# Performance work log

Hardware: AMD Instinct MI355X
Metric: run time of the kernel (lower is better)

The kernel has to match this reference:

```python
import jax, jax.numpy as jnp
import numpy as np

D = 131072   # input_dim = 2*256*256
H = 512      # lstm_hidden_dim
OUT = 128    # out_dim


def _lstm_cell(x, h, c, W_ih, W_hh, b_ih, b_hh):
    # PyTorch LSTMCell: gates in order (i, f, g, o)
    gates = x @ W_ih.T + b_ih + h @ W_hh.T + b_hh  # [1, 4H]
    i, f, g, o = jnp.split(gates, 4, axis=-1)
    i = jax.nn.sigmoid(i)
    f = jax.nn.sigmoid(f)
    g = jnp.tanh(g)
    o = jax.nn.sigmoid(o)
    c_new = f * c + i * g
    h_new = o * jnp.tanh(c_new)
    return h_new, c_new


def setup_inputs() -> dict:
    key = jax.random.key(0)
    ks = jax.random.split(key, 20)
    s_ih = 1.0 / np.sqrt(H)
    inp = {
        "dL_dU": jax.random.normal(ks[0], (256, 256), jnp.float32),
        "dL_dV": jax.random.normal(ks[1], (256, 256), jnp.float32),
        "hidden": jax.random.normal(ks[2], (2, 1, H), jnp.float32),
        "cell": jax.random.normal(ks[3], (2, 1, H), jnp.float32),
        "W_ih1": jax.random.uniform(ks[4], (4 * H, D), jnp.float32, -s_ih, s_ih),
        "W_hh1": jax.random.uniform(ks[5], (4 * H, H), jnp.float32, -s_ih, s_ih),
        "b_ih1": jax.random.uniform(ks[6], (4 * H,), jnp.float32, -s_ih, s_ih),
        "b_hh1": jax.random.uniform(ks[7], (4 * H,), jnp.float32, -s_ih, s_ih),
        "W_ih2": jax.random.uniform(ks[8], (4 * H, H), jnp.float32, -s_ih, s_ih),
        "W_hh2": jax.random.uniform(ks[9], (4 * H, H), jnp.float32, -s_ih, s_ih),
        "b_ih2": jax.random.uniform(ks[10], (4 * H,), jnp.float32, -s_ih, s_ih),
        "b_hh2": jax.random.uniform(ks[11], (4 * H,), jnp.float32, -s_ih, s_ih),
        "W1": jax.random.uniform(ks[12], (OUT * OUT, H), jnp.float32, -s_ih, s_ih),
        "b1": jax.random.uniform(ks[13], (OUT * OUT,), jnp.float32, -s_ih, s_ih),
        "W2": jax.random.uniform(ks[14], (1, H), jnp.float32, -s_ih, s_ih),
        "b2": jax.random.uniform(ks[15], (1,), jnp.float32, -s_ih, s_ih),
        "W3": jax.random.uniform(ks[16], (1, H), jnp.float32, -s_ih, s_ih),
        "b3": jax.random.uniform(ks[17], (1,), jnp.float32, -s_ih, s_ih),
    }
    return inp


def reference(dL_dU, dL_dV, hidden, cell,
              W_ih1, W_hh1, b_ih1, b_hh1,
              W_ih2, W_hh2, b_ih2, b_hh2,
              W1, b1, W2, b2, W3, b3):
    grad_flat = jnp.concatenate([dL_dU.reshape(-1), dL_dV.reshape(-1)], axis=0)[None, :]  # [1, D]
    h0, c0 = _lstm_cell(grad_flat, hidden[0], cell[0], W_ih1, W_hh1, b_ih1, b_hh1)
    h1, c1 = _lstm_cell(h0, hidden[1], cell[1], W_ih2, W_hh2, b_ih2, b_hh2)
    g = (h1 @ W1.T + b1).reshape(OUT, OUT)
    step_size = jnp.clip(h1 @ W2.T + b2, 1e-07, 0.005)
    m_c = jnp.clip(2.0 * jnp.clip(h0 @ W3.T + b3, 0.0, 1.0), 0.0, 1.0)
    return (g, step_size, m_c, jnp.stack((h0, h1)), jnp.stack((c0, c1)))
```

## Files before the change

kernel.cpp:

```cpp
#include <hip/hip_runtime.h>
#include <math.h>

#define D_IN 131072
#define H 512
#define G4 2048
#define OUTN 16384

#define OFF_STEP 16384
#define OFF_MC   16385
#define OFF_H0   16386
#define OFF_H1   16898
#define OFF_C0   17410
#define OFF_C1   17922

__device__ __forceinline__ float sigmoidf_(float x) {
    return 1.0f / (1.0f + __expf(-x));
}

__device__ __forceinline__ float dot4(float4 a, float4 b) {
    return a.x*b.x + a.y*b.y + a.z*b.z + a.w*b.w;
}

#define K1_ROWS 4
__global__ __launch_bounds__(1024) void k_gemv1(
    const float* __restrict__ U, const float* __restrict__ V,
    const float* __restrict__ Wih, const float* __restrict__ Whh,
    const float* __restrict__ bih, const float* __restrict__ bhh,
    const float* __restrict__ hidden, float* __restrict__ gates)
{
    __shared__ float4 xs[2048];
    __shared__ float red[16];
    const int tid  = threadIdx.x;
    const int wv   = tid >> 6;
    const int lane = tid & 63;
    const int rloc = wv >> 2;
    const int q    = wv & 3;
    const int row  = blockIdx.x * K1_ROWS + rloc;
    const float4* __restrict__ Wrow = (const float4*)(Wih + (size_t)row * D_IN);
    const float4* __restrict__ U4 = (const float4*)U;
    const float4* __restrict__ V4 = (const float4*)V;
    float acc = 0.0f;
    for (int c = 0; c < 16; ++c) {
        const float4* __restrict__ src = (c < 8) ? (U4 + (c << 11))
                                                 : (V4 + ((c - 8) << 11));
        __syncthreads();
        xs[tid]        = src[tid];
        xs[tid + 1024] = src[tid + 1024];
        __syncthreads();
        const float4* __restrict__ Wc = Wrow + (c << 11);
        const int base = (q << 9) + lane;
        #pragma unroll
        for (int k = 0; k < 8; ++k) {
            const int j = base + (k << 6);
            acc += dot4(Wc[j], xs[j]);
        }
    }
    if (q == 0) {
        const float4* __restrict__ Wh4 = (const float4*)(Whh + (size_t)row * H);
        const float4* h4 = (const float4*)hidden;
        acc += dot4(Wh4[lane], h4[lane]) + dot4(Wh4[lane + 64], h4[lane + 64]);
    }
    #pragma unroll
    for (int off = 32; off > 0; off >>= 1) acc += __shfl_down(acc, off);
    if (lane == 0) red[wv] = acc;
    __syncthreads();
    if (tid < K1_ROWS) {
        const int b = tid << 2;
        const int r = blockIdx.x * K1_ROWS + tid;
        gates[r] = red[b] + red[b+1] + red[b+2] + red[b+3] + bih[r] + bhh[r];
    }
}

__global__ __launch_bounds__(1024) void k_l2fused(
    const float* __restrict__ gates1, const float* __restrict__ cell_in,
    const float* __restrict__ hidden,
    const float* __restrict__ Wih2, const float* __restrict__ Whh2,
    const float* __restrict__ bih2, const float* __restrict__ bhh2,
    const float* __restrict__ W3, const float* __restrict__ b3,
    float* __restrict__ gates2, float* __restrict__ out)
{
    __shared__ float h0s[H];
    __shared__ float red[16];
    const int tid = threadIdx.x;
    if (tid < H) {
        float ig = sigmoidf_(gates1[tid]);
        float fg = sigmoidf_(gates1[H + tid]);
        float gg = tanhf(gates1[2*H + tid]);
        float og = sigmoidf_(gates1[3*H + tid]);
        float c  = fg * cell_in[tid] + ig * gg;
        float h  = og * tanhf(c);
        h0s[tid] = h;
        if (blockIdx.x == 0) {
            out[OFF_H0 + tid] = h;
            out[OFF_C0 + tid] = c;
        }
    }
    __syncthreads();
    const int wv = tid >> 6, lane = tid & 63;
    const int row = blockIdx.x * 16 + wv;
    const float4* __restrict__ Wr = (const float4*)(Wih2 + (size_t)row * H);
    const float4* __restrict__ Hr = (const float4*)(Whh2 + (size_t)row * H);
    const float4* h4 = (const float4*)h0s;
    const float4* __restrict__ y4 = (const float4*)(hidden + H);
    float acc = dot4(Wr[lane],      h4[lane])      + dot4(Hr[lane],      y4[lane])
              + dot4(Wr[lane + 64], h4[lane + 64]) + dot4(Hr[lane + 64], y4[lane + 64]);
    #pragma unroll
    for (int off = 32; off > 0; off >>= 1) acc += __shfl_down(acc, off);
    if (lane == 0) gates2[row] = acc + bih2[row] + bhh2[row];

    if (blockIdx.x == 0) {
        float p = (tid < H) ? h0s[tid] * W3[tid] : 0.0f;
        #pragma unroll
        for (int off = 32; off > 0; off >>= 1) p += __shfl_down(p, off);
        if (lane == 0) red[wv] = p;
        __syncthreads();
        if (tid == 0) {
            float v = b3[0];
            #pragma unroll
            for (int i = 0; i < 16; ++i) v += red[i];
            v = fminf(fmaxf(v, 0.0f), 1.0f);
            out[OFF_MC] = fminf(2.0f * v, 1.0f);
        }
    }
}

__global__ __launch_bounds__(512) void k_cell2(
    const float* __restrict__ gates2, const float* __restrict__ cell_in,
    const float* __restrict__ W2, const float* __restrict__ b2,
    float* __restrict__ h1, float* __restrict__ out)
{
    __shared__ float s[8];
    const int j = threadIdx.x;
    float ig = sigmoidf_(gates2[j]);
    float fg = sigmoidf_(gates2[H + j]);
    float gg = tanhf(gates2[2*H + j]);
    float og = sigmoidf_(gates2[3*H + j]);
    float c  = fg * cell_in[H + j] + ig * gg;
    float h  = og * tanhf(c);
    h1[j] = h;
    out[OFF_H1 + j] = h;
    out[OFF_C1 + j] = c;
    float p = h * W2[j];
    #pragma unroll
    for (int off = 32; off > 0; off >>= 1) p += __shfl_down(p, off);
    if ((j & 63) == 0) s[j >> 6] = p;
    __syncthreads();
    if (j == 0) {
        float v = s[0]+s[1]+s[2]+s[3]+s[4]+s[5]+s[6]+s[7] + b2[0];
        out[OFF_STEP] = fminf(fmaxf(v, 1e-7f), 0.005f);
    }
}

__global__ __launch_bounds__(256) void k_out_g(
    const float* __restrict__ W1, const float* __restrict__ b1,
    const float* __restrict__ h1, float* __restrict__ out)
{
    const int wave = (blockIdx.x * 256 + threadIdx.x) >> 6;
    const int lane = threadIdx.x & 63;
    const float4* __restrict__ Wr = (const float4*)(W1 + (size_t)wave * H);
    const float4* x4 = (const float4*)h1;
    float acc = dot4(Wr[lane], x4[lane]) + dot4(Wr[lane + 64], x4[lane + 64]);
    #pragma unroll
    for (int off = 32; off > 0; off >>= 1) acc += __shfl_down(acc, off);
    if (lane == 0) out[wave] = acc + b1[wave];
}

extern "C" void kernel_launch(void* const* d_in, const int* in_sizes, int n_in,
                              void* d_out, int out_size, void* d_ws, size_t ws_size,
                              hipStream_t stream) {
    const float* dL_dU  = (const float*)d_in[0];
    const float* dL_dV  = (const float*)d_in[1];
    const float* hidden = (const float*)d_in[2];
    const float* cell   = (const float*)d_in[3];
    const float* W_ih1  = (const float*)d_in[4];
    const float* W_hh1  = (const float*)d_in[5];
    const float* b_ih1  = (const float*)d_in[6];
    const float* b_hh1  = (const float*)d_in[7];
    const float* W_ih2  = (const float*)d_in[8];
    const float* W_hh2  = (const float*)d_in[9];
    const float* b_ih2  = (const float*)d_in[10];
    const float* b_hh2  = (const float*)d_in[11];
    const float* W1     = (const float*)d_in[12];
    const float* b1     = (const float*)d_in[13];
    const float* W2     = (const float*)d_in[14];
    const float* b2     = (const float*)d_in[15];
    const float* W3     = (const float*)d_in[16];
    const float* b3     = (const float*)d_in[17];

    float* out = (float*)d_out;
    float* ws  = (float*)d_ws;
    float* gates1 = ws;
    float* gates2 = ws + 2048;
    float* h1     = ws + 4096;

    k_gemv1<<<G4 / K1_ROWS, 1024, 0, stream>>>(dL_dU, dL_dV, W_ih1, W_hh1,
                                               b_ih1, b_hh1, hidden, gates1);
    k_l2fused<<<G4 / 16, 1024, 0, stream>>>(gates1, cell, hidden,
                                            W_ih2, W_hh2, b_ih2, b_hh2,
                                            W3, b3, gates2, out);
    k_cell2<<<1, 512, 0, stream>>>(gates2, cell, W2, b2, h1, out);
    k_out_g<<<OUTN / 4, 256, 0, stream>>>(W1, b1, h1, out);
    (void)in_sizes; (void)n_in; (void)out_size; (void)ws_size;
}
```

Measured before the change: 220.4 us.

## Split first-layer GEMV into K-sliced partials with 4-row register reuse

Replaces the single big GEMV kernel, which staged x in shared memory with block-wide barriers, by a split-K kernel. In it, each wave handles 4 rows times one 2048-float4 K slice, and each x load from global/L2 is reused across 4 rows in registers. A second small kernel reduces the 16 partials per row and adds the W_hh·h term and biases. This removes the shared-memory syncs and raises memory-level parallelism on the 1 GB weight stream, at the cost of an extra launch and a partials buffer.

```diff
diff --git a/kernel.cpp b/kernel.cpp
--- a/kernel.cpp
+++ b/kernel.cpp
@@ -5,6 +5,8 @@
 #define H 512
 #define G4 2048
 #define OUTN 16384
+#define NF4 32768
+#define KSLC 2048
 
 #define OFF_STEP 16384
 #define OFF_MC   16385
@@ -21,54 +23,61 @@
     return a.x*b.x + a.y*b.y + a.z*b.z + a.w*b.w;
 }
 
-#define K1_ROWS 4
-__global__ __launch_bounds__(1024) void k_gemv1(
+__global__ __launch_bounds__(256) void k_gemv1_part(
     const float* __restrict__ U, const float* __restrict__ V,
-    const float* __restrict__ Wih, const float* __restrict__ Whh,
-    const float* __restrict__ bih, const float* __restrict__ bhh,
-    const float* __restrict__ hidden, float* __restrict__ gates)
-{
-    __shared__ float4 xs[2048];
-    __shared__ float red[16];
-    const int tid  = threadIdx.x;
-    const int wv   = tid >> 6;
-    const int lane = tid & 63;
-    const int rloc = wv >> 2;
-    const int q    = wv & 3;
-    const int row  = blockIdx.x * K1_ROWS + rloc;
-    const float4* __restrict__ Wrow = (const float4*)(Wih + (size_t)row * D_IN);
-    const float4* __restrict__ U4 = (const float4*)U;
-    const float4* __restrict__ V4 = (const float4*)V;
-    float acc = 0.0f;
-    for (int c = 0; c < 16; ++c) {
-        const float4* __restrict__ src = (c < 8) ? (U4 + (c << 11))
-                                                 : (V4 + ((c - 8) << 11));
-        __syncthreads();
-        xs[tid]        = src[tid];
-        xs[tid + 1024] = src[tid + 1024];
-        __syncthreads();
-        const float4* __restrict__ Wc = Wrow + (c << 11);
-        const int base = (q << 9) + lane;
-        #pragma unroll
-        for (int k = 0; k < 8; ++k) {
-            const int j = base + (k << 6);
-            acc += dot4(Wc[j], xs[j]);
-        }
-    }
-    if (q == 0) {
-        const float4* __restrict__ Wh4 = (const float4*)(Whh + (size_t)row * H);
-        const float4* h4 = (const float4*)hidden;
-        acc += dot4(Wh4[lane], h4[lane]) + dot4(Wh4[lane + 64], h4[lane + 64]);
-    }
+    const float* __restrict__ Wih, float* __restrict__ partial)
+{
+    const int wg   = blockIdx.x * 4 + (threadIdx.x >> 6);
+    const int lane = threadIdx.x & 63;
+    const int rg   = wg >> 4;
+    const int ks   = wg & 15;
+    const float4* __restrict__ xs =
+        (ks < 8) ? ((const float4*)U + (ks << 11))
+                 : ((const float4*)V + ((ks - 8) << 11));
+    const float4* __restrict__ W0 =
+        (const float4*)Wih + (size_t)(rg * 4) * NF4 + (ks << 11);
+    const float4* __restrict__ W1r = W0 + NF4;
+    const float4* __restrict__ W2r = W1r + NF4;
+    const float4* __restrict__ W3r = W2r + NF4;
+    float a0 = 0.f, a1 = 0.f, a2 = 0.f, a3 = 0.f;
+    #pragma unroll 2
+    for (int i = lane; i < KSLC; i += 64) {
+        float4 xv = xs[i];
+        a0 += dot4(W0[i], xv);
+        a1 += dot4(W1r[i], xv);
+        a2 += dot4(W2r[i], xv);
+        a3 += dot4(W3r[i], xv);
+    }
+    #pragma unroll
+    for (int off = 32; off > 0; off >>= 1) {
+        a0 += __shfl_down(a0, off);
+        a1 += __shfl_down(a1, off);
+        a2 += __shfl_down(a2, off);
+        a3 += __shfl_down(a3, off);
+    }
+    if (lane == 0) {
+        float* p = partial + (size_t)(rg * 4) * 16 + ks;
+        p[0]  = a0;
+        p[16] = a1;
+        p[32] = a2;
+        p[48] = a3;
+    }
+}
+
+__global__ __launch_bounds__(256) void k_gemv1_comb(
+    const float* __restrict__ partial, const float* __restrict__ Whh,
+    const float* __restrict__ hidden, const float* __restrict__ bih,
+    const float* __restrict__ bhh, float* __restrict__ gates)
+{
+    const int r    = (blockIdx.x * 256 + threadIdx.x) >> 6;
+    const int lane = threadIdx.x & 63;
+    const float4* __restrict__ Wh = (const float4*)(Whh + (size_t)r * H);
+    const float4* h4 = (const float4*)hidden;
+    float acc = dot4(Wh[lane], h4[lane]) + dot4(Wh[lane + 64], h4[lane + 64]);
+    if (lane < 16) acc += partial[r * 16 + lane];
     #pragma unroll
     for (int off = 32; off > 0; off >>= 1) acc += __shfl_down(acc, off);
-    if (lane == 0) red[wv] = acc;
-    __syncthreads();
-    if (tid < K1_ROWS) {
-        const int b = tid << 2;
-        const int r = blockIdx.x * K1_ROWS + tid;
-        gates[r] = red[b] + red[b+1] + red[b+2] + red[b+3] + bih[r] + bhh[r];
-    }
+    if (lane == 0) gates[r] = acc + bih[r] + bhh[r];
 }
 
 __global__ __launch_bounds__(1024) void k_l2fused(
@@ -189,12 +198,14 @@
 
     float* out = (float*)d_out;
     float* ws  = (float*)d_ws;
-    float* gates1 = ws;
-    float* gates2 = ws + 2048;
-    float* h1     = ws + 4096;
-
-    k_gemv1<<<G4 / K1_ROWS, 1024, 0, stream>>>(dL_dU, dL_dV, W_ih1, W_hh1,
-                                               b_ih1, b_hh1, hidden, gates1);
+    float* partial = ws;
+    float* gates1  = ws + 32768;
+    float* gates2  = ws + 32768 + 2048;
+    float* h1      = ws + 32768 + 4096;
+
+    k_gemv1_part<<<2048, 256, 0, stream>>>(dL_dU, dL_dV, W_ih1, partial);
+    k_gemv1_comb<<<512, 256, 0, stream>>>(partial, W_hh1, hidden,
+                                          b_ih1, b_hh1, gates1);
     k_l2fused<<<G4 / 16, 1024, 0, stream>>>(gates1, cell, hidden,
                                             W_ih2, W_hh2, b_ih2, b_hh2,
                                             W3, b3, gates2, out);
```

Measured after the change: 219.2 us. Within noise of the previous version (-0.6%).

## Restructure layer-1 GEMV to one row per block with nontemporal weight loads

Applied to the files above, without the earlier changes.

The large W_ih1 GEMV now assigns one output row to each 256-thread block. Each block streams its row directly against the input vector read from global memory, so the shared-memory staging and its per-chunk barriers are gone. All weight loads in the GEMV kernels use nontemporal loads so the single-use weight stream does not evict the reused input vectors from cache. The trade-off is more blocks, and the input vector is now fetched from L2/global by every block instead of being shared across four rows per block.

```diff
diff --git a/kernel.cpp b/kernel.cpp
--- a/kernel.cpp
+++ b/kernel.cpp
@@ -21,53 +21,45 @@
     return a.x*b.x + a.y*b.y + a.z*b.z + a.w*b.w;
 }
 
-#define K1_ROWS 4
-__global__ __launch_bounds__(1024) void k_gemv1(
+typedef float f4v __attribute__((ext_vector_type(4)));
+__device__ __forceinline__ float4 ntload4(const float4* p) {
+    f4v v = __builtin_nontemporal_load((const f4v*)p);
+    float4 r; r.x = v.x; r.y = v.y; r.z = v.z; r.w = v.w;
+    return r;
+}
+
+__global__ __launch_bounds__(256) void k_gemv1(
     const float* __restrict__ U, const float* __restrict__ V,
     const float* __restrict__ Wih, const float* __restrict__ Whh,
     const float* __restrict__ bih, const float* __restrict__ bhh,
     const float* __restrict__ hidden, float* __restrict__ gates)
 {
-    __shared__ float4 xs[2048];
-    __shared__ float red[16];
-    const int tid  = threadIdx.x;
-    const int wv   = tid >> 6;
-    const int lane = tid & 63;
-    const int rloc = wv >> 2;
-    const int q    = wv & 3;
-    const int row  = blockIdx.x * K1_ROWS + rloc;
-    const float4* __restrict__ Wrow = (const float4*)(Wih + (size_t)row * D_IN);
+    const int r = blockIdx.x;
+    const int t = threadIdx.x;
+    const float4* __restrict__ Wrow = (const float4*)(Wih + (size_t)r * D_IN);
     const float4* __restrict__ U4 = (const float4*)U;
     const float4* __restrict__ V4 = (const float4*)V;
     float acc = 0.0f;
-    for (int c = 0; c < 16; ++c) {
-        const float4* __restrict__ src = (c < 8) ? (U4 + (c << 11))
-                                                 : (V4 + ((c - 8) << 11));
-        __syncthreads();
-        xs[tid]        = src[tid];
-        xs[tid + 1024] = src[tid + 1024];
-        __syncthreads();
-        const float4* __restrict__ Wc = Wrow + (c << 11);
-        const int base = (q << 9) + lane;
-        #pragma unroll
-        for (int k = 0; k < 8; ++k) {
-            const int j = base + (k << 6);
-            acc += dot4(Wc[j], xs[j]);
-        }
+    #pragma unroll 4
+    for (int idx = t; idx < 16384; idx += 256) {
+        acc += dot4(ntload4(&Wrow[idx]), U4[idx]);
     }
-    if (q == 0) {
-        const float4* __restrict__ Wh4 = (const float4*)(Whh + (size_t)row * H);
-        const float4* h4 = (const float4*)hidden;
-        acc += dot4(Wh4[lane], h4[lane]) + dot4(Wh4[lane + 64], h4[lane + 64]);
+    #pragma unroll 4
+    for (int idx = t; idx < 16384; idx += 256) {
+        acc += dot4(ntload4(&Wrow[idx + 16384]), V4[idx]);
+    }
+    if (t < 128) {
+        const float4* Wh4 = (const float4*)(Whh + (size_t)r * H);
+        const float4* h4  = (const float4*)hidden;
+        acc += dot4(ntload4(&Wh4[t]), h4[t]);
     }
     #pragma unroll
     for (int off = 32; off > 0; off >>= 1) acc += __shfl_down(acc, off);
-    if (lane == 0) red[wv] = acc;
+    __shared__ float s[4];
+    if ((t & 63) == 0) s[t >> 6] = acc;
     __syncthreads();
-    if (tid < K1_ROWS) {
-        const int b = tid << 2;
-        const int r = blockIdx.x * K1_ROWS + tid;
-        gates[r] = red[b] + red[b+1] + red[b+2] + red[b+3] + bih[r] + bhh[r];
+    if (t == 0) {
+        gates[r] = s[0] + s[1] + s[2] + s[3] + bih[r] + bhh[r];
     }
 }
 
@@ -102,8 +94,10 @@
     const float4* __restrict__ Hr = (const float4*)(Whh2 + (size_t)row * H);
     const float4* h4 = (const float4*)h0s;
     const float4* __restrict__ y4 = (const float4*)(hidden + H);
-    float acc = dot4(Wr[lane],      h4[lane])      + dot4(Hr[lane],      y4[lane])
-              + dot4(Wr[lane + 64], h4[lane + 64]) + dot4(Hr[lane + 64], y4[lane + 64]);
+    float acc = dot4(ntload4(&Wr[lane]),      h4[lane])
+              + dot4(ntload4(&Hr[lane]),      y4[lane])
+              + dot4(ntload4(&Wr[lane + 64]), h4[lane + 64])
+              + dot4(ntload4(&Hr[lane + 64]), y4[lane + 64]);
     #pragma unroll
     for (int off = 32; off > 0; off >>= 1) acc += __shfl_down(acc, off);
     if (lane == 0) gates2[row] = acc + bih2[row] + bhh2[row];
@@ -159,7 +153,8 @@
     const int lane = threadIdx.x & 63;
     const float4* __restrict__ Wr = (const float4*)(W1 + (size_t)wave * H);
     const float4* x4 = (const float4*)h1;
-    float acc = dot4(Wr[lane], x4[lane]) + dot4(Wr[lane + 64], x4[lane + 64]);
+    float acc = dot4(ntload4(&Wr[lane]),      x4[lane])
+              + dot4(ntload4(&Wr[lane + 64]), x4[lane + 64]);
     #pragma unroll
     for (int off = 32; off > 0; off >>= 1) acc += __shfl_down(acc, off);
     if (lane == 0) out[wave] = acc + b1[wave];
@@ -193,8 +188,8 @@
     float* gates2 = ws + 2048;
     float* h1     = ws + 4096;
 
-    k_gemv1<<<G4 / K1_ROWS, 1024, 0, stream>>>(dL_dU, dL_dV, W_ih1, W_hh1,
-                                               b_ih1, b_hh1, hidden, gates1);
+    k_gemv1<<<G4, 256, 0, stream>>>(dL_dU, dL_dV, W_ih1, W_hh1, b_ih1, b_hh1,
+                                    hidden, gates1);
     k_l2fused<<<G4 / 16, 1024, 0, stream>>>(gates1, cell, hidden,
                                             W_ih2, W_hh2, b_ih2, b_hh2,
                                             W3, b3, gates2, out);
```

After: 195.1 us. -11.5%, faster.
